# Kernel optimization log

Hardware: AMD Instinct MI355X
Metric: run time of the kernel (lower is better)

## Reference

```python
import jax, jax.numpy as jnp
import numpy as np

N_NODES = 100000
N_EDGES = 1_600_000
D_IN = 128
D_OUT = 128


def setup_inputs() -> dict:
    key = jax.random.key(0)
    k1, k2, k3 = jax.random.split(key, 3)
    input_matrix = jax.random.normal(k1, (N_NODES, D_IN), dtype=jnp.float32)
    adjacency_coo_matrix = jax.random.randint(k2, (2, N_EDGES), 0, N_NODES, dtype=jnp.int64)
    # xavier-uniform-style init for the weight matrix
    limit = float(np.sqrt(6.0 / (D_IN + D_OUT)))
    weights_matrix = jax.random.uniform(k3, (D_IN, D_OUT), dtype=jnp.float32, minval=-limit, maxval=limit)
    return {
        "input_matrix": input_matrix,
        "adjacency_coo_matrix": adjacency_coo_matrix,
        "weights_matrix": weights_matrix,
    }


def reference(input_matrix, adjacency_coo_matrix, weights_matrix):
    # Edge-wise gathers (the irregular-access pattern from the torch code)
    src_idx = adjacency_coo_matrix[0]
    dst_idx = adjacency_coo_matrix[1]
    neighbors = input_matrix[dst_idx]  # [E, D_IN] gather of neighbor features
    # Mean-aggregate neighbor features onto each src node
    agg = jax.ops.segment_sum(neighbors, src_idx, num_segments=N_NODES)  # [N, D_IN]
    deg = jax.ops.segment_sum(jnp.ones((neighbors.shape[0],), dtype=input_matrix.dtype),
                              src_idx, num_segments=N_NODES)  # [N]
    mean_agg = agg / jnp.maximum(deg, 1.0)[:, None]
    # Linear transform with the layer weight matrix
    out = mean_agg @ weights_matrix  # [N, D_OUT]
    return out
```

## Files before the change

### kernel.cpp

```cpp
#include <hip/hip_runtime.h>

#define NN 100000
#define NE 1600000
#define DD 128
#define CAP 64
#define SLICE_N 12500
#define FILL_BLOCKS 2048
#define BPS (FILL_BLOCKS / 8)
#define GEMM_BLOCKS ((NN + 63) / 64)
#define LDSP 136

typedef __bf16 bf16x8 __attribute__((ext_vector_type(8)));
typedef float  f32x4  __attribute__((ext_vector_type(4)));

__device__ __forceinline__ unsigned int f2bf(float f) {
    unsigned int u = __float_as_uint(f);
    return (u + 0x7FFFu + ((u >> 16) & 1u)) >> 16;
}
__device__ __forceinline__ float bflo(unsigned int u) { return __uint_as_float(u << 16); }
__device__ __forceinline__ float bfhi(unsigned int u) { return __uint_as_float(u & 0xFFFF0000u); }

__global__ __launch_bounds__(256) void k_prep(const float* __restrict__ W,
                                              unsigned short* __restrict__ wtb,
                                              int* __restrict__ cnt)
{
    const int idx = blockIdx.x * 256 + (int)threadIdx.x;
    const int k = idx >> 7, n = idx & 127;
    wtb[n * DD + k] = (unsigned short)f2bf(W[idx]);
    int4* c4 = (int4*)cnt;
    for (int i = idx; i < NN / 4; i += DD * DD) c4[i] = make_int4(0, 0, 0, 0);
}

__global__ __launch_bounds__(256, 8) void k_fused(const int* __restrict__ adj,
                                                  int* __restrict__ cnt,
                                                  int* __restrict__ edge_dst,
                                                  const float* __restrict__ x,
                                                  const unsigned short* __restrict__ wtb,
                                                  unsigned short* __restrict__ y)
{
    __shared__ unsigned short ytile[64 * LDSP];

    const int b = blockIdx.x;

    {
        const int slice = b & 7;
        const int w     = b >> 3;
        const int lo    = slice * SLICE_N;
        const uint4* src4 = (const uint4*)adj;
        const uint4* dst4 = (const uint4*)(adj + NE);
        const int ngroups = NE / 4;
        const int stride  = BPS * 256;

        for (int g = w * 256 + (int)threadIdx.x; g < ngroups; g += stride) {
            const uint4 s4 = src4[g];
            const uint4 d4 = dst4[g];
            const int sv[4] = {(int)s4.x, (int)s4.y, (int)s4.z, (int)s4.w};
            const int dv[4] = {(int)d4.x, (int)d4.y, (int)d4.z, (int)d4.w};
            int slot[4];
            #pragma unroll
            for (int j = 0; j < 4; ++j) {
                slot[j] = ((unsigned)(sv[j] - lo) < (unsigned)SLICE_N)
                          ? atomicAdd(&cnt[sv[j]], 1) : CAP;
            }
            #pragma unroll
            for (int j = 0; j < 4; ++j) {
                if (slot[j] < CAP)
                    edge_dst[(size_t)sv[j] * CAP + slot[j]] = dv[j];
            }
        }
    }

    if (b >= GEMM_BLOCKS) return;

    const int wave = (int)threadIdx.x >> 6;
    const int lane = (int)threadIdx.x & 63;
    const int quad = lane >> 4;
    const int l16  = lane & 15;
    const int mbase = b * 64 + wave * 16;
    const int m = mbase + l16;

    bf16x8 a[4];
    if (m < NN) {
        const float* arow = x + (size_t)m * DD + quad * 8;
        #pragma unroll
        for (int ks = 0; ks < 4; ++ks) {
            const float4 f0 = *(const float4*)(arow + ks * 32);
            const float4 f1 = *(const float4*)(arow + ks * 32 + 4);
            uint4 p;
            p.x = f2bf(f0.x) | (f2bf(f0.y) << 16);
            p.y = f2bf(f0.z) | (f2bf(f0.w) << 16);
            p.z = f2bf(f1.x) | (f2bf(f1.y) << 16);
            p.w = f2bf(f1.z) | (f2bf(f1.w) << 16);
            a[ks] = __builtin_bit_cast(bf16x8, p);
        }
    } else {
        const uint4 z = make_uint4(0, 0, 0, 0);
        #pragma unroll
        for (int ks = 0; ks < 4; ++ks) a[ks] = __builtin_bit_cast(bf16x8, z);
    }

    unsigned short* lrow = ytile + wave * 16 * LDSP;

    #pragma unroll
    for (int nt = 0; nt < 8; ++nt) {
        f32x4 c = {0.f, 0.f, 0.f, 0.f};
        const unsigned short* bcol = wtb + (nt * 16 + l16) * DD + quad * 8;
        #pragma unroll
        for (int ks = 0; ks < 4; ++ks) {
            const bf16x8 bb = __builtin_bit_cast(bf16x8, *(const uint4*)(bcol + ks * 32));
            c = __builtin_amdgcn_mfma_f32_16x16x32_bf16(a[ks], bb, c, 0, 0, 0);
        }
        #pragma unroll
        for (int r = 0; r < 4; ++r)
            lrow[(quad * 4 + r) * LDSP + nt * 16 + l16] = (unsigned short)f2bf(c[r]);
    }

    __syncthreads();

    const int r16  = lane >> 2;
    const int ch   = lane & 3;
    const int grow = mbase - l16 + ( (lane >> 2) );
    const int growr = b * 64 + wave * 16 + r16;
    if (growr < NN) {
        const unsigned short* lsrc = ytile + (wave * 16 + r16) * LDSP + ch * 32;
        unsigned short* gdst = y + (size_t)growr * DD + ch * 32;
        const uint4 q0 = *(const uint4*)(lsrc + 0);
        const uint4 q1 = *(const uint4*)(lsrc + 8);
        const uint4 q2 = *(const uint4*)(lsrc + 16);
        const uint4 q3 = *(const uint4*)(lsrc + 24);
        *(uint4*)(gdst + 0)  = q0;
        *(uint4*)(gdst + 8)  = q1;
        *(uint4*)(gdst + 16) = q2;
        *(uint4*)(gdst + 24) = q3;
    }
    (void)grow; (void)r16;
}

__global__ __launch_bounds__(256) void k_agg2(const unsigned short* __restrict__ y,
                                              const int* __restrict__ cnt,
                                              const int* __restrict__ edge_dst,
                                              float* __restrict__ out)
{
    const int n    = blockIdx.x * 4 + ((int)threadIdx.x >> 6);
    const int lane = (int)threadIdx.x & 63;
    const int eg   = lane >> 4;
    const int h    = lane & 15;
    int deg = cnt[n];
    if (deg > CAP) deg = CAP;
    const int* el = edge_dst + (size_t)n * CAP;

    float acc[8] = {0.f,0.f,0.f,0.f,0.f,0.f,0.f,0.f};

    #define ACC(p) do {                                         \
        acc[0] += bflo((p).x); acc[1] += bfhi((p).x);           \
        acc[2] += bflo((p).y); acc[3] += bfhi((p).y);           \
        acc[4] += bflo((p).z); acc[5] += bfhi((p).z);           \
        acc[6] += bflo((p).w); acc[7] += bfhi((p).w);           \
    } while (0)

    int i = eg;
    for (; i + 12 < deg; i += 16) {
        const int d0 = el[i];
        const int d1 = el[i + 4];
        const int d2 = el[i + 8];
        const int d3 = el[i + 12];
        const uint4 p0 = *(const uint4*)(y + (size_t)d0 * DD + h * 8);
        const uint4 p1 = *(const uint4*)(y + (size_t)d1 * DD + h * 8);
        const uint4 p2 = *(const uint4*)(y + (size_t)d2 * DD + h * 8);
        const uint4 p3 = *(const uint4*)(y + (size_t)d3 * DD + h * 8);
        ACC(p0); ACC(p1); ACC(p2); ACC(p3);
    }
    for (; i + 4 < deg; i += 8) {
        const int d0 = el[i];
        const int d1 = el[i + 4];
        const uint4 p0 = *(const uint4*)(y + (size_t)d0 * DD + h * 8);
        const uint4 p1 = *(const uint4*)(y + (size_t)d1 * DD + h * 8);
        ACC(p0); ACC(p1);
    }
    for (; i < deg; i += 4) {
        const int d0 = el[i];
        const uint4 p0 = *(const uint4*)(y + (size_t)d0 * DD + h * 8);
        ACC(p0);
    }
    #undef ACC

    #pragma unroll
    for (int j = 0; j < 8; ++j) {
        acc[j] += __shfl_xor(acc[j], 16, 64);
        acc[j] += __shfl_xor(acc[j], 32, 64);
    }

    if (eg == 0) {
        const float inv = 1.0f / fmaxf((float)deg, 1.0f);
        float* o = out + (size_t)n * DD + h * 8;
        float4 w0 = {acc[0]*inv, acc[1]*inv, acc[2]*inv, acc[3]*inv};
        float4 w1 = {acc[4]*inv, acc[5]*inv, acc[6]*inv, acc[7]*inv};
        *(float4*)(o + 0) = w0;
        *(float4*)(o + 4) = w1;
    }
}

extern "C" void kernel_launch(void* const* d_in, const int* in_sizes, int n_in,
                              void* d_out, int out_size, void* d_ws, size_t ws_size,
                              hipStream_t stream) {
    const float* x   = (const float*)d_in[0];
    const int*   adj = (const int*)d_in[1];
    const float* W   = (const float*)d_in[2];
    float* out = (float*)d_out;

    unsigned short* y   = (unsigned short*)d_ws;
    unsigned short* wtb = y + (size_t)NN * DD;
    int* cnt      = (int*)(wtb + DD * DD);
    int* edge_dst = cnt + NN;

    k_prep <<<DD * DD / 256, 256, 0, stream>>>(W, wtb, cnt);
    k_fused<<<FILL_BLOCKS, 256, 0, stream>>>(adj, cnt, edge_dst, x, wtb, y);
    k_agg2 <<<NN / 4, 256, 0, stream>>>(y, cnt, edge_dst, out);
}
```

Measured before the change: 252.2 us.

## Split fill and GEMM kernels, stage in-slice edges in LDS queue before atomics

The fused fill+GEMM kernel becomes two separate kernels. The fill kernel now compacts in-slice edges with wave ballots into an LDS queue and issues the global count atomics in a batched phase at the end, so atomic issue is decoupled from the streaming loads. Adjacency and feature reads use nontemporal loads. The split removes the overlap between the fill and GEMM work and adds a launch, while the queue adds LDS pressure and extra syncs.

```diff
diff --git a/kernel.cpp b/kernel.cpp
--- a/kernel.cpp
+++ b/kernel.cpp
@@ -7,11 +7,13 @@
 #define SLICE_N 12500
 #define FILL_BLOCKS 2048
 #define BPS (FILL_BLOCKS / 8)
+#define QCAP 1024
 #define GEMM_BLOCKS ((NN + 63) / 64)
 #define LDSP 136
 
 typedef __bf16 bf16x8 __attribute__((ext_vector_type(8)));
 typedef float  f32x4  __attribute__((ext_vector_type(4)));
+typedef unsigned int u32x4 __attribute__((ext_vector_type(4)));
 
 __device__ __forceinline__ unsigned int f2bf(float f) {
     unsigned int u = __float_as_uint(f);
@@ -31,47 +33,84 @@
     for (int i = idx; i < NN / 4; i += DD * DD) c4[i] = make_int4(0, 0, 0, 0);
 }
 
-__global__ __launch_bounds__(256, 8) void k_fused(const int* __restrict__ adj,
-                                                  int* __restrict__ cnt,
-                                                  int* __restrict__ edge_dst,
-                                                  const float* __restrict__ x,
-                                                  const unsigned short* __restrict__ wtb,
-                                                  unsigned short* __restrict__ y)
-{
-    __shared__ unsigned short ytile[64 * LDSP];
-
-    const int b = blockIdx.x;
-
-    {
-        const int slice = b & 7;
-        const int w     = b >> 3;
-        const int lo    = slice * SLICE_N;
-        const uint4* src4 = (const uint4*)adj;
-        const uint4* dst4 = (const uint4*)(adj + NE);
-        const int ngroups = NE / 4;
-        const int stride  = BPS * 256;
-
-        for (int g = w * 256 + (int)threadIdx.x; g < ngroups; g += stride) {
-            const uint4 s4 = src4[g];
-            const uint4 d4 = dst4[g];
-            const int sv[4] = {(int)s4.x, (int)s4.y, (int)s4.z, (int)s4.w};
-            const int dv[4] = {(int)d4.x, (int)d4.y, (int)d4.z, (int)d4.w};
-            int slot[4];
-            #pragma unroll
-            for (int j = 0; j < 4; ++j) {
-                slot[j] = ((unsigned)(sv[j] - lo) < (unsigned)SLICE_N)
-                          ? atomicAdd(&cnt[sv[j]], 1) : CAP;
-            }
-            #pragma unroll
-            for (int j = 0; j < 4; ++j) {
-                if (slot[j] < CAP)
-                    edge_dst[(size_t)sv[j] * CAP + slot[j]] = dv[j];
+__global__ __launch_bounds__(256, 8) void k_fill(const int* __restrict__ adj,
+                                                 int* __restrict__ cnt,
+                                                 int* __restrict__ edge_dst)
+{
+    __shared__ int2 q[QCAP];
+    __shared__ int qn;
+    if (threadIdx.x == 0) qn = 0;
+    __syncthreads();
+
+    const int slice = blockIdx.x & 7;
+    const int w     = blockIdx.x >> 3;
+    const int lo    = slice * SLICE_N;
+    const int lane  = (int)threadIdx.x & 63;
+    const unsigned long long ltmask = (1ull << lane) - 1ull;
+    const u32x4* src4 = (const u32x4*)adj;
+    const u32x4* dst4 = (const u32x4*)(adj + NE);
+    const int ngroups = NE / 4;
+    const int stride  = BPS * 256;
+
+    for (int g = w * 256 + (int)threadIdx.x; g < ngroups; g += stride) {
+        const u32x4 s4 = __builtin_nontemporal_load(src4 + g);
+        const u32x4 d4 = __builtin_nontemporal_load(dst4 + g);
+        #pragma unroll
+        for (int j = 0; j < 4; ++j) {
+            const int s = (int)s4[j];
+            const int d = (int)d4[j];
+            const bool pred = ((unsigned)(s - lo) < (unsigned)SLICE_N);
+            const unsigned long long m = __ballot(pred);
+            if (m) {
+                const int ldr = (int)__ffsll(m) - 1;
+                int base = 0;
+                if (lane == ldr) base = atomicAdd(&qn, (int)__popcll(m));
+                base = __shfl(base, ldr, 64);
+                if (pred) {
+                    const int pos = base + (int)__popcll(m & ltmask);
+                    if (pos < QCAP) {
+                        q[pos] = make_int2(s, d);
+                    } else {
+                        const int slot = atomicAdd(&cnt[s], 1);
+                        if (slot < CAP) edge_dst[(size_t)s * CAP + slot] = d;
+                    }
+                }
             }
         }
     }
 
-    if (b >= GEMM_BLOCKS) return;
-
+    __syncthreads();
+    int total = qn;
+    if (total > QCAP) total = QCAP;
+
+    const int t = (int)threadIdx.x;
+    const bool v0 = (t       < total);
+    const bool v1 = (t + 256 < total);
+    const bool v2 = (t + 512 < total);
+    const bool v3 = (t + 768 < total);
+    int2 e0, e1, e2, e3;
+    if (v0) e0 = q[t];
+    if (v1) e1 = q[t + 256];
+    if (v2) e2 = q[t + 512];
+    if (v3) e3 = q[t + 768];
+    int a0 = CAP, a1 = CAP, a2 = CAP, a3 = CAP;
+    if (v0) a0 = atomicAdd(&cnt[e0.x], 1);
+    if (v1) a1 = atomicAdd(&cnt[e1.x], 1);
+    if (v2) a2 = atomicAdd(&cnt[e2.x], 1);
+    if (v3) a3 = atomicAdd(&cnt[e3.x], 1);
+    if (v0 && a0 < CAP) edge_dst[(size_t)e0.x * CAP + a0] = e0.y;
+    if (v1 && a1 < CAP) edge_dst[(size_t)e1.x * CAP + a1] = e1.y;
+    if (v2 && a2 < CAP) edge_dst[(size_t)e2.x * CAP + a2] = e2.y;
+    if (v3 && a3 < CAP) edge_dst[(size_t)e3.x * CAP + a3] = e3.y;
+}
+
+__global__ __launch_bounds__(256, 8) void k_gemm(const float* __restrict__ x,
+                                                 const unsigned short* __restrict__ wtb,
+                                                 unsigned short* __restrict__ y)
+{
+    __shared__ unsigned short ytile[64 * LDSP];
+
+    const int b    = blockIdx.x;
     const int wave = (int)threadIdx.x >> 6;
     const int lane = (int)threadIdx.x & 63;
     const int quad = lane >> 4;
@@ -84,17 +123,17 @@
         const float* arow = x + (size_t)m * DD + quad * 8;
         #pragma unroll
         for (int ks = 0; ks < 4; ++ks) {
-            const float4 f0 = *(const float4*)(arow + ks * 32);
-            const float4 f1 = *(const float4*)(arow + ks * 32 + 4);
-            uint4 p;
-            p.x = f2bf(f0.x) | (f2bf(f0.y) << 16);
-            p.y = f2bf(f0.z) | (f2bf(f0.w) << 16);
-            p.z = f2bf(f1.x) | (f2bf(f1.y) << 16);
-            p.w = f2bf(f1.z) | (f2bf(f1.w) << 16);
+            const f32x4 f0 = __builtin_nontemporal_load((const f32x4*)(arow + ks * 32));
+            const f32x4 f1 = __builtin_nontemporal_load((const f32x4*)(arow + ks * 32 + 4));
+            u32x4 p;
+            p[0] = f2bf(f0[0]) | (f2bf(f0[1]) << 16);
+            p[1] = f2bf(f0[2]) | (f2bf(f0[3]) << 16);
+            p[2] = f2bf(f1[0]) | (f2bf(f1[1]) << 16);
+            p[3] = f2bf(f1[2]) | (f2bf(f1[3]) << 16);
             a[ks] = __builtin_bit_cast(bf16x8, p);
         }
     } else {
-        const uint4 z = make_uint4(0, 0, 0, 0);
+        const u32x4 z = 0;
         #pragma unroll
         for (int ks = 0; ks < 4; ++ks) a[ks] = __builtin_bit_cast(bf16x8, z);
     }
@@ -119,7 +158,6 @@
 
     const int r16  = lane >> 2;
     const int ch   = lane & 3;
-    const int grow = mbase - l16 + ( (lane >> 2) );
     const int growr = b * 64 + wave * 16 + r16;
     if (growr < NN) {
         const unsigned short* lsrc = ytile + (wave * 16 + r16) * LDSP + ch * 32;
@@ -133,7 +171,6 @@
         *(uint4*)(gdst + 16) = q2;
         *(uint4*)(gdst + 24) = q3;
     }
-    (void)grow; (void)r16;
 }
 
 __global__ __launch_bounds__(256) void k_agg2(const unsigned short* __restrict__ y,
@@ -213,7 +250,8 @@
     int* cnt      = (int*)(wtb + DD * DD);
     int* edge_dst = cnt + NN;
 
-    k_prep <<<DD * DD / 256, 256, 0, stream>>>(W, wtb, cnt);
-    k_fused<<<FILL_BLOCKS, 256, 0, stream>>>(adj, cnt, edge_dst, x, wtb, y);
-    k_agg2 <<<NN / 4, 256, 0, stream>>>(y, cnt, edge_dst, out);
-}
+    k_prep<<<DD * DD / 256, 256, 0, stream>>>(W, wtb, cnt);
+    k_fill<<<FILL_BLOCKS, 256, 0, stream>>>(adj, cnt, edge_dst);
+    k_gemm<<<GEMM_BLOCKS, 256, 0, stream>>>(x, wtb, y);
+    k_agg2<<<NN / 4, 256, 0, stream>>>(y, cnt, edge_dst, out);
+}
```

After: 276.8 us. 9.7% more time.

## Replace per-node atomic CSR fill with coarse binning and in-LDS sort-aggregate

Applied to the files above, without the earlier changes.

Edges are now scattered into bins of 32 source nodes with one atomic per edge on a bin counter, replacing the old scheme where 8 slice passes each rescanned the whole edge list. A new aggregation kernel counts and sorts each bin's edges in LDS, then gathers rows of the transformed features per node. The weight transpose moves into LDS inside the fused bin+GEMM kernel, and memset replaces the prep kernel. The risk is dropped edges if a bin holds more than 1024 entries, plus more atomic contention per bin.

```diff
diff --git a/kernel.cpp b/kernel.cpp
--- a/kernel.cpp
+++ b/kernel.cpp
@@ -3,15 +3,16 @@
 #define NN 100000
 #define NE 1600000
 #define DD 128
-#define CAP 64
-#define SLICE_N 12500
-#define FILL_BLOCKS 2048
-#define BPS (FILL_BLOCKS / 8)
-#define GEMM_BLOCKS ((NN + 63) / 64)
+#define BINW 32
+#define NBIN (NN / BINW)
+#define BCAP 1024
+#define NGRP (NE / 4)
+#define KAB ((NGRP + 255) / 256)
 #define LDSP 136
 
 typedef __bf16 bf16x8 __attribute__((ext_vector_type(8)));
 typedef float  f32x4  __attribute__((ext_vector_type(4)));
+typedef unsigned int u32x4 __attribute__((ext_vector_type(4)));
 
 __device__ __forceinline__ unsigned int f2bf(float f) {
     unsigned int u = __float_as_uint(f);
@@ -20,60 +21,43 @@
 __device__ __forceinline__ float bflo(unsigned int u) { return __uint_as_float(u << 16); }
 __device__ __forceinline__ float bfhi(unsigned int u) { return __uint_as_float(u & 0xFFFF0000u); }
 
-__global__ __launch_bounds__(256) void k_prep(const float* __restrict__ W,
-                                              unsigned short* __restrict__ wtb,
-                                              int* __restrict__ cnt)
-{
-    const int idx = blockIdx.x * 256 + (int)threadIdx.x;
-    const int k = idx >> 7, n = idx & 127;
-    wtb[n * DD + k] = (unsigned short)f2bf(W[idx]);
-    int4* c4 = (int4*)cnt;
-    for (int i = idx; i < NN / 4; i += DD * DD) c4[i] = make_int4(0, 0, 0, 0);
-}
-
-__global__ __launch_bounds__(256, 8) void k_fused(const int* __restrict__ adj,
-                                                  int* __restrict__ cnt,
-                                                  int* __restrict__ edge_dst,
+__global__ __launch_bounds__(256) void k_bin_gemm(const int* __restrict__ adj,
+                                                  int* __restrict__ gcnt,
+                                                  int2* __restrict__ binbuf,
                                                   const float* __restrict__ x,
-                                                  const unsigned short* __restrict__ wtb,
+                                                  const float* __restrict__ W,
                                                   unsigned short* __restrict__ y)
 {
+    __shared__ unsigned short wtb_s[DD * LDSP];
     __shared__ unsigned short ytile[64 * LDSP];
 
-    const int b = blockIdx.x;
+    const int b   = (int)blockIdx.x;
+    const int tid = (int)threadIdx.x;
 
     {
-        const int slice = b & 7;
-        const int w     = b >> 3;
-        const int lo    = slice * SLICE_N;
-        const uint4* src4 = (const uint4*)adj;
-        const uint4* dst4 = (const uint4*)(adj + NE);
-        const int ngroups = NE / 4;
-        const int stride  = BPS * 256;
-
-        for (int g = w * 256 + (int)threadIdx.x; g < ngroups; g += stride) {
-            const uint4 s4 = src4[g];
-            const uint4 d4 = dst4[g];
-            const int sv[4] = {(int)s4.x, (int)s4.y, (int)s4.z, (int)s4.w};
-            const int dv[4] = {(int)d4.x, (int)d4.y, (int)d4.z, (int)d4.w};
-            int slot[4];
+        const int g = b * 256 + tid;
+        if (g < NGRP) {
+            const u32x4 s4 = __builtin_nontemporal_load((const u32x4*)adj + g);
+            const u32x4 d4 = __builtin_nontemporal_load((const u32x4*)(adj + NE) + g);
+            int pos[4];
             #pragma unroll
-            for (int j = 0; j < 4; ++j) {
-                slot[j] = ((unsigned)(sv[j] - lo) < (unsigned)SLICE_N)
-                          ? atomicAdd(&cnt[sv[j]], 1) : CAP;
-            }
+            for (int j = 0; j < 4; ++j)
+                pos[j] = atomicAdd(&gcnt[(int)s4[j] >> 5], 1);
             #pragma unroll
-            for (int j = 0; j < 4; ++j) {
-                if (slot[j] < CAP)
-                    edge_dst[(size_t)sv[j] * CAP + slot[j]] = dv[j];
-            }
-        }
-    }
-
-    if (b >= GEMM_BLOCKS) return;
-
-    const int wave = (int)threadIdx.x >> 6;
-    const int lane = (int)threadIdx.x & 63;
+            for (int j = 0; j < 4; ++j)
+                if (pos[j] < BCAP)
+                    binbuf[((int)s4[j] >> 5) * BCAP + pos[j]] = make_int2((int)s4[j], (int)d4[j]);
+        }
+    }
+
+    for (int i = tid; i < DD * DD; i += 256) {
+        const int k = i >> 7, n = i & 127;
+        wtb_s[n * LDSP + k] = (unsigned short)f2bf(W[i]);
+    }
+    __syncthreads();
+
+    const int wave = tid >> 6;
+    const int lane = tid & 63;
     const int quad = lane >> 4;
     const int l16  = lane & 15;
     const int mbase = b * 64 + wave * 16;
@@ -84,17 +68,17 @@
         const float* arow = x + (size_t)m * DD + quad * 8;
         #pragma unroll
         for (int ks = 0; ks < 4; ++ks) {
-            const float4 f0 = *(const float4*)(arow + ks * 32);
-            const float4 f1 = *(const float4*)(arow + ks * 32 + 4);
-            uint4 p;
-            p.x = f2bf(f0.x) | (f2bf(f0.y) << 16);
-            p.y = f2bf(f0.z) | (f2bf(f0.w) << 16);
-            p.z = f2bf(f1.x) | (f2bf(f1.y) << 16);
-            p.w = f2bf(f1.z) | (f2bf(f1.w) << 16);
+            const f32x4 f0 = __builtin_nontemporal_load((const f32x4*)(arow + ks * 32));
+            const f32x4 f1 = __builtin_nontemporal_load((const f32x4*)(arow + ks * 32 + 4));
+            u32x4 p;
+            p[0] = f2bf(f0[0]) | (f2bf(f0[1]) << 16);
+            p[1] = f2bf(f0[2]) | (f2bf(f0[3]) << 16);
+            p[2] = f2bf(f1[0]) | (f2bf(f1[1]) << 16);
+            p[3] = f2bf(f1[2]) | (f2bf(f1[3]) << 16);
             a[ks] = __builtin_bit_cast(bf16x8, p);
         }
     } else {
-        const uint4 z = make_uint4(0, 0, 0, 0);
+        const u32x4 z = 0;
         #pragma unroll
         for (int ks = 0; ks < 4; ++ks) a[ks] = __builtin_bit_cast(bf16x8, z);
     }
@@ -104,7 +88,7 @@
     #pragma unroll
     for (int nt = 0; nt < 8; ++nt) {
         f32x4 c = {0.f, 0.f, 0.f, 0.f};
-        const unsigned short* bcol = wtb + (nt * 16 + l16) * DD + quad * 8;
+        const unsigned short* bcol = wtb_s + (nt * 16 + l16) * LDSP + quad * 8;
         #pragma unroll
         for (int ks = 0; ks < 4; ++ks) {
             const bf16x8 bb = __builtin_bit_cast(bf16x8, *(const uint4*)(bcol + ks * 32));
@@ -117,39 +101,62 @@
 
     __syncthreads();
 
-    const int r16  = lane >> 2;
-    const int ch   = lane & 3;
-    const int grow = mbase - l16 + ( (lane >> 2) );
+    const int r16   = lane >> 2;
+    const int ch    = lane & 3;
     const int growr = b * 64 + wave * 16 + r16;
     if (growr < NN) {
         const unsigned short* lsrc = ytile + (wave * 16 + r16) * LDSP + ch * 32;
         unsigned short* gdst = y + (size_t)growr * DD + ch * 32;
-        const uint4 q0 = *(const uint4*)(lsrc + 0);
-        const uint4 q1 = *(const uint4*)(lsrc + 8);
-        const uint4 q2 = *(const uint4*)(lsrc + 16);
-        const uint4 q3 = *(const uint4*)(lsrc + 24);
-        *(uint4*)(gdst + 0)  = q0;
-        *(uint4*)(gdst + 8)  = q1;
-        *(uint4*)(gdst + 16) = q2;
-        *(uint4*)(gdst + 24) = q3;
-    }
-    (void)grow; (void)r16;
-}
-
-__global__ __launch_bounds__(256) void k_agg2(const unsigned short* __restrict__ y,
-                                              const int* __restrict__ cnt,
-                                              const int* __restrict__ edge_dst,
-                                              float* __restrict__ out)
+        *(uint4*)(gdst + 0)  = *(const uint4*)(lsrc + 0);
+        *(uint4*)(gdst + 8)  = *(const uint4*)(lsrc + 8);
+        *(uint4*)(gdst + 16) = *(const uint4*)(lsrc + 16);
+        *(uint4*)(gdst + 24) = *(const uint4*)(lsrc + 24);
+    }
+}
+
+__global__ __launch_bounds__(256) void k_sortagg(const int2* __restrict__ binbuf,
+                                                 const int* __restrict__ gcnt,
+                                                 const unsigned short* __restrict__ y,
+                                                 float* __restrict__ out)
 {
-    const int n    = blockIdx.x * 4 + ((int)threadIdx.x >> 6);
-    const int lane = (int)threadIdx.x & 63;
+    __shared__ int scnt[BINW];
+    __shared__ int soff[BINW];
+    __shared__ int scur[BINW];
+    __shared__ int sdst[BCAP];
+
+    const int b   = (int)blockIdx.x;
+    const int tid = (int)threadIdx.x;
+    const int lo  = b * BINW;
+    int ne = gcnt[b];
+    if (ne > BCAP) ne = BCAP;
+    const int2* eb = binbuf + (size_t)b * BCAP;
+
+    if (tid < BINW) scnt[tid] = 0;
+    __syncthreads();
+
+    for (int e = tid; e < ne; e += 256)
+        atomicAdd(&scnt[eb[e].x - lo], 1);
+    __syncthreads();
+
+    if (tid < BINW) {
+        int a = 0;
+        for (int j = 0; j < tid; ++j) a += scnt[j];
+        soff[tid] = a;
+        scur[tid] = a;
+    }
+    __syncthreads();
+
+    for (int e = tid; e < ne; e += 256) {
+        const int2 ed = eb[e];
+        const int p = atomicAdd(&scur[ed.x - lo], 1);
+        sdst[p] = ed.y;
+    }
+    __syncthreads();
+
+    const int wave = tid >> 6;
+    const int lane = tid & 63;
     const int eg   = lane >> 4;
     const int h    = lane & 15;
-    int deg = cnt[n];
-    if (deg > CAP) deg = CAP;
-    const int* el = edge_dst + (size_t)n * CAP;
-
-    float acc[8] = {0.f,0.f,0.f,0.f,0.f,0.f,0.f,0.f};
 
     #define ACC(p) do {                                         \
         acc[0] += bflo((p).x); acc[1] += bfhi((p).x);           \
@@ -158,46 +165,39 @@
         acc[6] += bflo((p).w); acc[7] += bfhi((p).w);           \
     } while (0)
 
-    int i = eg;
-    for (; i + 12 < deg; i += 16) {
-        const int d0 = el[i];
-        const int d1 = el[i + 4];
-        const int d2 = el[i + 8];
-        const int d3 = el[i + 12];
-        const uint4 p0 = *(const uint4*)(y + (size_t)d0 * DD + h * 8);
-        const uint4 p1 = *(const uint4*)(y + (size_t)d1 * DD + h * 8);
-        const uint4 p2 = *(const uint4*)(y + (size_t)d2 * DD + h * 8);
-        const uint4 p3 = *(const uint4*)(y + (size_t)d3 * DD + h * 8);
-        ACC(p0); ACC(p1); ACC(p2); ACC(p3);
-    }
-    for (; i + 4 < deg; i += 8) {
-        const int d0 = el[i];
-        const int d1 = el[i + 4];
-        const uint4 p0 = *(const uint4*)(y + (size_t)d0 * DD + h * 8);
-        const uint4 p1 = *(const uint4*)(y + (size_t)d1 * DD + h * 8);
-        ACC(p0); ACC(p1);
-    }
-    for (; i < deg; i += 4) {
-        const int d0 = el[i];
-        const uint4 p0 = *(const uint4*)(y + (size_t)d0 * DD + h * 8);
-        ACC(p0);
-    }
-    #undef ACC
-
     #pragma unroll
-    for (int j = 0; j < 8; ++j) {
-        acc[j] += __shfl_xor(acc[j], 16, 64);
-        acc[j] += __shfl_xor(acc[j], 32, 64);
-    }
-
-    if (eg == 0) {
+    for (int jj = 0; jj < 2; ++jj) {
+        const int j   = wave * 8 + jj * 4 + eg;
+        const int deg = scnt[j];
+        const int st  = soff[j];
+        float acc[8] = {0.f,0.f,0.f,0.f,0.f,0.f,0.f,0.f};
+
+        int i = 0;
+        for (; i + 3 < deg; i += 4) {
+            const int d0 = sdst[st + i];
+            const int d1 = sdst[st + i + 1];
+            const int d2 = sdst[st + i + 2];
+            const int d3 = sdst[st + i + 3];
+            const uint4 p0 = *(const uint4*)(y + (size_t)d0 * DD + h * 8);
+            const uint4 p1 = *(const uint4*)(y + (size_t)d1 * DD + h * 8);
+            const uint4 p2 = *(const uint4*)(y + (size_t)d2 * DD + h * 8);
+            const uint4 p3 = *(const uint4*)(y + (size_t)d3 * DD + h * 8);
+            ACC(p0); ACC(p1); ACC(p2); ACC(p3);
+        }
+        for (; i < deg; ++i) {
+            const int d0 = sdst[st + i];
+            const uint4 p0 = *(const uint4*)(y + (size_t)d0 * DD + h * 8);
+            ACC(p0);
+        }
+
         const float inv = 1.0f / fmaxf((float)deg, 1.0f);
-        float* o = out + (size_t)n * DD + h * 8;
+        float* o = out + (size_t)(lo + j) * DD + h * 8;
         float4 w0 = {acc[0]*inv, acc[1]*inv, acc[2]*inv, acc[3]*inv};
         float4 w1 = {acc[4]*inv, acc[5]*inv, acc[6]*inv, acc[7]*inv};
         *(float4*)(o + 0) = w0;
         *(float4*)(o + 4) = w1;
     }
+    #undef ACC
 }
 
 extern "C" void kernel_launch(void* const* d_in, const int* in_sizes, int n_in,
@@ -208,12 +208,11 @@
     const float* W   = (const float*)d_in[2];
     float* out = (float*)d_out;
 
-    unsigned short* y   = (unsigned short*)d_ws;
-    unsigned short* wtb = y + (size_t)NN * DD;
-    int* cnt      = (int*)(wtb + DD * DD);
-    int* edge_dst = cnt + NN;
-
-    k_prep <<<DD * DD / 256, 256, 0, stream>>>(W, wtb, cnt);
-    k_fused<<<FILL_BLOCKS, 256, 0, stream>>>(adj, cnt, edge_dst, x, wtb, y);
-    k_agg2 <<<NN / 4, 256, 0, stream>>>(y, cnt, edge_dst, out);
-}
+    unsigned short* y = (unsigned short*)d_ws;
+    int2* binbuf = (int2*)(y + (size_t)NN * DD);
+    int*  gcnt   = (int*)(binbuf + (size_t)NBIN * BCAP);
+
+    hipMemsetAsync(gcnt, 0, NBIN * sizeof(int), stream);
+    k_bin_gemm<<<KAB, 256, 0, stream>>>(adj, gcnt, binbuf, x, W, y);
+    k_sortagg<<<NBIN, 256, 0, stream>>>(binbuf, gcnt, y, out);
+}
```

New measurement: 314.2 us. +24.6%, slower.

## Assign one node per 16-lane group in aggregation and use nontemporal streaming loads

Applied to the files above, without the earlier changes.

The aggregation kernel now gives each 16-lane group of a wave its own node, where before a whole wave split one node's edges four ways. Each group walks its node's edge list serially with 8-way unrolled gathers, which removes the cross-lane shuffle reduction and the idle-lane stores, and the grid shrinks fourfold. The fill phase and the x loads now use nontemporal loads and stores so streamed data pollutes the cache less. The cost is that nodes with different degrees in one wave cause divergence, and per-group memory-level parallelism differs from before.

```diff
diff --git a/kernel.cpp b/kernel.cpp
--- a/kernel.cpp
+++ b/kernel.cpp
@@ -7,11 +7,13 @@
 #define SLICE_N 12500
 #define FILL_BLOCKS 2048
 #define BPS (FILL_BLOCKS / 8)
+#define NGRP (NE / 4)
 #define GEMM_BLOCKS ((NN + 63) / 64)
 #define LDSP 136
 
 typedef __bf16 bf16x8 __attribute__((ext_vector_type(8)));
 typedef float  f32x4  __attribute__((ext_vector_type(4)));
+typedef unsigned int u32x4 __attribute__((ext_vector_type(4)));
 
 __device__ __forceinline__ unsigned int f2bf(float f) {
     unsigned int u = __float_as_uint(f);
@@ -40,23 +42,23 @@
 {
     __shared__ unsigned short ytile[64 * LDSP];
 
-    const int b = blockIdx.x;
+    const int b   = (int)blockIdx.x;
+    const int tid = (int)threadIdx.x;
 
     {
         const int slice = b & 7;
         const int w     = b >> 3;
         const int lo    = slice * SLICE_N;
-        const uint4* src4 = (const uint4*)adj;
-        const uint4* dst4 = (const uint4*)(adj + NE);
-        const int ngroups = NE / 4;
+        const u32x4* src4 = (const u32x4*)adj;
+        const u32x4* dst4 = (const u32x4*)(adj + NE);
         const int stride  = BPS * 256;
 
-        for (int g = w * 256 + (int)threadIdx.x; g < ngroups; g += stride) {
-            const uint4 s4 = src4[g];
-            const uint4 d4 = dst4[g];
-            const int sv[4] = {(int)s4.x, (int)s4.y, (int)s4.z, (int)s4.w};
-            const int dv[4] = {(int)d4.x, (int)d4.y, (int)d4.z, (int)d4.w};
-            int slot[4];
+        for (int g = w * 256 + tid; g < NGRP; g += stride) {
+            const u32x4 s4 = __builtin_nontemporal_load(src4 + g);
+            const u32x4 d4 = __builtin_nontemporal_load(dst4 + g);
+            int sv[4], dv[4], slot[4];
+            #pragma unroll
+            for (int j = 0; j < 4; ++j) { sv[j] = (int)s4[j]; dv[j] = (int)d4[j]; }
             #pragma unroll
             for (int j = 0; j < 4; ++j) {
                 slot[j] = ((unsigned)(sv[j] - lo) < (unsigned)SLICE_N)
@@ -65,15 +67,16 @@
             #pragma unroll
             for (int j = 0; j < 4; ++j) {
                 if (slot[j] < CAP)
-                    edge_dst[(size_t)sv[j] * CAP + slot[j]] = dv[j];
+                    __builtin_nontemporal_store(dv[j],
+                        edge_dst + (size_t)sv[j] * CAP + slot[j]);
             }
         }
     }
 
     if (b >= GEMM_BLOCKS) return;
 
-    const int wave = (int)threadIdx.x >> 6;
-    const int lane = (int)threadIdx.x & 63;
+    const int wave = tid >> 6;
+    const int lane = tid & 63;
     const int quad = lane >> 4;
     const int l16  = lane & 15;
     const int mbase = b * 64 + wave * 16;
@@ -84,17 +87,17 @@
         const float* arow = x + (size_t)m * DD + quad * 8;
         #pragma unroll
         for (int ks = 0; ks < 4; ++ks) {
-            const float4 f0 = *(const float4*)(arow + ks * 32);
-            const float4 f1 = *(const float4*)(arow + ks * 32 + 4);
-            uint4 p;
-            p.x = f2bf(f0.x) | (f2bf(f0.y) << 16);
-            p.y = f2bf(f0.z) | (f2bf(f0.w) << 16);
-            p.z = f2bf(f1.x) | (f2bf(f1.y) << 16);
-            p.w = f2bf(f1.z) | (f2bf(f1.w) << 16);
+            const f32x4 f0 = __builtin_nontemporal_load((const f32x4*)(arow + ks * 32));
+            const f32x4 f1 = __builtin_nontemporal_load((const f32x4*)(arow + ks * 32 + 4));
+            u32x4 p;
+            p[0] = f2bf(f0[0]) | (f2bf(f0[1]) << 16);
+            p[1] = f2bf(f0[2]) | (f2bf(f0[3]) << 16);
+            p[2] = f2bf(f1[0]) | (f2bf(f1[1]) << 16);
+            p[3] = f2bf(f1[2]) | (f2bf(f1[3]) << 16);
             a[ks] = __builtin_bit_cast(bf16x8, p);
         }
     } else {
-        const uint4 z = make_uint4(0, 0, 0, 0);
+        const u32x4 z = 0;
         #pragma unroll
         for (int ks = 0; ks < 4; ++ks) a[ks] = __builtin_bit_cast(bf16x8, z);
     }
@@ -117,34 +120,31 @@
 
     __syncthreads();
 
-    const int r16  = lane >> 2;
-    const int ch   = lane & 3;
-    const int grow = mbase - l16 + ( (lane >> 2) );
+    const int r16   = lane >> 2;
+    const int ch    = lane & 3;
     const int growr = b * 64 + wave * 16 + r16;
     if (growr < NN) {
         const unsigned short* lsrc = ytile + (wave * 16 + r16) * LDSP + ch * 32;
         unsigned short* gdst = y + (size_t)growr * DD + ch * 32;
-        const uint4 q0 = *(const uint4*)(lsrc + 0);
-        const uint4 q1 = *(const uint4*)(lsrc + 8);
-        const uint4 q2 = *(const uint4*)(lsrc + 16);
-        const uint4 q3 = *(const uint4*)(lsrc + 24);
-        *(uint4*)(gdst + 0)  = q0;
-        *(uint4*)(gdst + 8)  = q1;
-        *(uint4*)(gdst + 16) = q2;
-        *(uint4*)(gdst + 24) = q3;
-    }
-    (void)grow; (void)r16;
-}
-
-__global__ __launch_bounds__(256) void k_agg2(const unsigned short* __restrict__ y,
+        *(uint4*)(gdst + 0)  = *(const uint4*)(lsrc + 0);
+        *(uint4*)(gdst + 8)  = *(const uint4*)(lsrc + 8);
+        *(uint4*)(gdst + 16) = *(const uint4*)(lsrc + 16);
+        *(uint4*)(gdst + 24) = *(const uint4*)(lsrc + 24);
+    }
+}
+
+__global__ __launch_bounds__(256) void k_agg3(const unsigned short* __restrict__ y,
                                               const int* __restrict__ cnt,
                                               const int* __restrict__ edge_dst,
                                               float* __restrict__ out)
 {
-    const int n    = blockIdx.x * 4 + ((int)threadIdx.x >> 6);
-    const int lane = (int)threadIdx.x & 63;
+    const int tid  = (int)threadIdx.x;
+    const int wave = tid >> 6;
+    const int lane = tid & 63;
     const int eg   = lane >> 4;
     const int h    = lane & 15;
+    const int n    = (int)blockIdx.x * 16 + wave * 4 + eg;
+
     int deg = cnt[n];
     if (deg > CAP) deg = CAP;
     const int* el = edge_dst + (size_t)n * CAP;
@@ -158,46 +158,51 @@
         acc[6] += bflo((p).w); acc[7] += bfhi((p).w);           \
     } while (0)
 
-    int i = eg;
-    for (; i + 12 < deg; i += 16) {
+    int i = 0;
+    for (; i + 7 < deg; i += 8) {
         const int d0 = el[i];
-        const int d1 = el[i + 4];
-        const int d2 = el[i + 8];
-        const int d3 = el[i + 12];
+        const int d1 = el[i + 1];
+        const int d2 = el[i + 2];
+        const int d3 = el[i + 3];
+        const int d4 = el[i + 4];
+        const int d5 = el[i + 5];
+        const int d6 = el[i + 6];
+        const int d7 = el[i + 7];
+        const uint4 p0 = *(const uint4*)(y + (size_t)d0 * DD + h * 8);
+        const uint4 p1 = *(const uint4*)(y + (size_t)d1 * DD + h * 8);
+        const uint4 p2 = *(const uint4*)(y + (size_t)d2 * DD + h * 8);
+        const uint4 p3 = *(const uint4*)(y + (size_t)d3 * DD + h * 8);
+        const uint4 p4 = *(const uint4*)(y + (size_t)d4 * DD + h * 8);
+        const uint4 p5 = *(const uint4*)(y + (size_t)d5 * DD + h * 8);
+        const uint4 p6 = *(const uint4*)(y + (size_t)d6 * DD + h * 8);
+        const uint4 p7 = *(const uint4*)(y + (size_t)d7 * DD + h * 8);
+        ACC(p0); ACC(p1); ACC(p2); ACC(p3);
+        ACC(p4); ACC(p5); ACC(p6); ACC(p7);
+    }
+    for (; i + 3 < deg; i += 4) {
+        const int d0 = el[i];
+        const int d1 = el[i + 1];
+        const int d2 = el[i + 2];
+        const int d3 = el[i + 3];
         const uint4 p0 = *(const uint4*)(y + (size_t)d0 * DD + h * 8);
         const uint4 p1 = *(const uint4*)(y + (size_t)d1 * DD + h * 8);
         const uint4 p2 = *(const uint4*)(y + (size_t)d2 * DD + h * 8);
         const uint4 p3 = *(const uint4*)(y + (size_t)d3 * DD + h * 8);
         ACC(p0); ACC(p1); ACC(p2); ACC(p3);
     }
-    for (; i + 4 < deg; i += 8) {
-        const int d0 = el[i];
-        const int d1 = el[i + 4];
-        const uint4 p0 = *(const uint4*)(y + (size_t)d0 * DD + h * 8);
-        const uint4 p1 = *(const uint4*)(y + (size_t)d1 * DD + h * 8);
-        ACC(p0); ACC(p1);
-    }
-    for (; i < deg; i += 4) {
+    for (; i < deg; ++i) {
         const int d0 = el[i];
         const uint4 p0 = *(const uint4*)(y + (size_t)d0 * DD + h * 8);
         ACC(p0);
     }
     #undef ACC
 
-    #pragma unroll
-    for (int j = 0; j < 8; ++j) {
-        acc[j] += __shfl_xor(acc[j], 16, 64);
-        acc[j] += __shfl_xor(acc[j], 32, 64);
-    }
-
-    if (eg == 0) {
-        const float inv = 1.0f / fmaxf((float)deg, 1.0f);
-        float* o = out + (size_t)n * DD + h * 8;
-        float4 w0 = {acc[0]*inv, acc[1]*inv, acc[2]*inv, acc[3]*inv};
-        float4 w1 = {acc[4]*inv, acc[5]*inv, acc[6]*inv, acc[7]*inv};
-        *(float4*)(o + 0) = w0;
-        *(float4*)(o + 4) = w1;
-    }
+    const float inv = 1.0f / fmaxf((float)deg, 1.0f);
+    float* o = out + (size_t)n * DD + h * 8;
+    float4 w0 = {acc[0]*inv, acc[1]*inv, acc[2]*inv, acc[3]*inv};
+    float4 w1 = {acc[4]*inv, acc[5]*inv, acc[6]*inv, acc[7]*inv};
+    *(float4*)(o + 0) = w0;
+    *(float4*)(o + 4) = w1;
 }
 
 extern "C" void kernel_launch(void* const* d_in, const int* in_sizes, int n_in,
@@ -215,5 +220,5 @@
 
     k_prep <<<DD * DD / 256, 256, 0, stream>>>(W, wtb, cnt);
     k_fused<<<FILL_BLOCKS, 256, 0, stream>>>(adj, cnt, edge_dst, x, wtb, y);
-    k_agg2 <<<NN / 4, 256, 0, stream>>>(y, cnt, edge_dst, out);
-}
+    k_agg3 <<<NN / 16, 256, 0, stream>>>(y, cnt, edge_dst, out);
+}
```

New measurement: 266.6 us. 5.7% more time.
